# Optimization experiments

Measured on AMD Instinct MI355X. Metric: run time of the kernel, lower is better.

The kernel has to match this reference:

```python
import jax, jax.numpy as jnp
import numpy as np

D_MODEL = 1024
NUM_HEADS = 16
HEAD_DIM = D_MODEL // NUM_HEADS


def setup_inputs() -> dict:
    key = jax.random.key(0)
    ks = jax.random.split(key, 11)
    S, B, D = 2048, 2, D_MODEL
    scale = 1.0 / np.sqrt(D)
    inp = {
        'query': jax.random.normal(ks[0], (S, B, D), dtype=jnp.float32),
        'key': jax.random.normal(ks[1], (S, B, D), dtype=jnp.float32),
        'value': jax.random.normal(ks[2], (S, B, D), dtype=jnp.float32),
        'Wq': jax.random.normal(ks[3], (D, D), dtype=jnp.float32) * scale,
        'bq': jnp.zeros((D,), dtype=jnp.float32),
        'Wk': jax.random.normal(ks[4], (D, D), dtype=jnp.float32) * scale,
        'bk': jnp.zeros((D,), dtype=jnp.float32),
        'Wv': jax.random.normal(ks[5], (D, D), dtype=jnp.float32) * scale,
        'bv': jnp.zeros((D,), dtype=jnp.float32),
        'Wo': jax.random.normal(ks[6], (D, D), dtype=jnp.float32) * scale,
        'bo': jnp.zeros((D,), dtype=jnp.float32),
    }
    return inp


def reference(query, key, value, Wq, bq, Wk, bk, Wv, bv, Wo, bo):
    # query/key/value: [S, B, D] (seq-first, as in the torch module)
    S, B, D = query.shape
    H, Hd = NUM_HEADS, HEAD_DIM
    # Linear: x @ W.T + b (torch convention), then split heads -> [B, H, S, Hd]
    def proj_heads(x, W, b):
        y = jnp.einsum('sbd,ed->sbe', x, W) + b  # [S, B, D]
        return y.reshape(x.shape[0], B, H, Hd).transpose(1, 2, 0, 3)
    q = proj_heads(query, Wq, bq)   # [B, H, S, Hd]
    k = proj_heads(key, Wk, bk)     # [B, H, Sk, Hd]
    v = proj_heads(value, Wv, bv)   # [B, H, Sk, Hd]
    scores = jnp.einsum('bhsd,bhtd->bhst', q, k) / jnp.sqrt(jnp.asarray(Hd, q.dtype))
    probs = jax.nn.softmax(scores, axis=-1)  # dropout p=0.0 -> identity
    attn = jnp.einsum('bhst,bhtd->bhsd', probs, v)  # [B, H, S, Hd]
    attn = attn.transpose(2, 0, 1, 3).reshape(S, B, D)  # [S, B, D]
    out = jnp.einsum('sbd,ed->sbe', attn, Wo) + bo
    return out
```

## Files before the change

kernel.cpp:

```cpp
#include <hip/hip_runtime.h>
#include <stdint.h>

#define S_LEN 2048
#define BATCH 2
#define DM    1024
#define NH    16
#define HD    64
#define MROWS 4096

typedef float f32x4 __attribute__((ext_vector_type(4)));
typedef short bfrag __attribute__((ext_vector_type(8)));
typedef unsigned short u16x4_t __attribute__((ext_vector_type(4)));
typedef unsigned short u16x8_t __attribute__((ext_vector_type(8)));
typedef int i32x4_t __attribute__((ext_vector_type(4)));

#define EXP2F(x) __builtin_amdgcn_exp2f(x)

__device__ inline f32x4 mfma16(bfrag a, bfrag b, f32x4 c) {
    return __builtin_amdgcn_mfma_f32_16x16x32_bf16(a, b, c, 0, 0, 0);
}

__device__ inline unsigned short bf16_rn(float x) {
    unsigned u = __builtin_bit_cast(unsigned, x);
    return (unsigned short)((u + 0x7fffu + ((u >> 16) & 1u)) >> 16);
}

__device__ inline void split_bf16(float x, unsigned short &h, unsigned short &l) {
    unsigned u = __builtin_bit_cast(unsigned, x);
    h = (unsigned short)(u >> 16);
    float hf = __builtin_bit_cast(float, u & 0xffff0000u);
    float r = x - hf;
    l = (unsigned short)(__builtin_bit_cast(unsigned, r) >> 16);
}

__device__ inline unsigned cvtpk_bf16(float lo, float hi) {
    unsigned r;
    asm("v_cvt_pk_bf16_f32 %0, %1, %2" : "=v"(r) : "v"(lo), "v"(hi));
    return r;
}

__device__ inline void pl32swap(unsigned &a, unsigned &b) {
    asm("v_permlane32_swap_b32 %0, %1" : "+v"(a), "+v"(b));
}
__device__ inline void pl16swap(unsigned &a, unsigned &b) {
    asm("v_permlane16_swap_b32 %0, %1" : "+v"(a), "+v"(b));
}

typedef __attribute__((address_space(1))) const unsigned int as1_u32;
typedef __attribute__((address_space(3))) unsigned int as3_u32;
__device__ inline void async16(void* lds, const void* g) {
    __builtin_amdgcn_global_load_lds((as1_u32*)g, (as3_u32*)lds, 16, 0, 0);
}

__global__ __launch_bounds__(256)
void cvt_kernel(const float* __restrict__ Wq, const float* __restrict__ Wk,
                const float* __restrict__ Wv, const float* __restrict__ Wo,
                const float* __restrict__ Qin, const float* __restrict__ Kin,
                const float* __restrict__ Vin,
                unsigned short* __restrict__ Wqb, unsigned short* __restrict__ Wkb,
                unsigned short* __restrict__ Wvb,
                unsigned short* __restrict__ Woh, unsigned short* __restrict__ Wol,
                unsigned short* __restrict__ Qa,  unsigned short* __restrict__ Ka,
                unsigned short* __restrict__ Va)
{
    const int z = blockIdx.z;
    size_t idx = ((size_t)blockIdx.x * 256 + threadIdx.x) * 8;
    const size_t limit = (z < 4) ? (size_t)DM * DM : (size_t)MROWS * DM;
    if (idx >= limit) return;
    const float* src = (z == 0) ? Wq : (z == 1) ? Wk : (z == 2) ? Wv :
                       (z == 3) ? Wo : (z == 4) ? Qin : (z == 5) ? Kin : Vin;
    float4 f0 = *(const float4*)&src[idx];
    float4 f1 = *(const float4*)&src[idx + 4];
    if (z != 3) {
        unsigned short* dst = (z == 0) ? Wqb : (z == 1) ? Wkb : (z == 2) ? Wvb :
                              (z == 4) ? Qa  : (z == 5) ? Ka  : Va;
        u16x8_t v = { bf16_rn(f0.x), bf16_rn(f0.y), bf16_rn(f0.z), bf16_rn(f0.w),
                      bf16_rn(f1.x), bf16_rn(f1.y), bf16_rn(f1.z), bf16_rn(f1.w) };
        *(u16x8_t*)&dst[idx] = v;
    } else {
        unsigned short h0,h1,h2,h3,h4,h5,h6,h7, l0,l1,l2,l3,l4,l5,l6,l7;
        split_bf16(f0.x,h0,l0); split_bf16(f0.y,h1,l1);
        split_bf16(f0.z,h2,l2); split_bf16(f0.w,h3,l3);
        split_bf16(f1.x,h4,l4); split_bf16(f1.y,h5,l5);
        split_bf16(f1.z,h6,l6); split_bf16(f1.w,h7,l7);
        u16x8_t vh = {h0,h1,h2,h3,h4,h5,h6,h7};
        u16x8_t vl = {l0,l1,l2,l3,l4,l5,l6,l7};
        *(u16x8_t*)&Woh[idx] = vh;
        *(u16x8_t*)&Wol[idx] = vl;
    }
}

__global__ __launch_bounds__(256)
void qkv_gemm(const unsigned short* __restrict__ Qa,
              const unsigned short* __restrict__ Ka,
              const unsigned short* __restrict__ Va,
              const unsigned short* __restrict__ Wqb,
              const unsigned short* __restrict__ Wkb,
              const unsigned short* __restrict__ Wvb,
              const float* __restrict__ bq, const float* __restrict__ bk,
              const float* __restrict__ bv,
              unsigned short* __restrict__ Qb, unsigned short* __restrict__ Kb,
              unsigned short* __restrict__ Vt)
{
    __shared__ unsigned short sA[128*32];
    __shared__ unsigned short sB[128*32];

    const int tid = threadIdx.x, lane = tid & 63, w4 = tid >> 6;
    const int m16 = lane & 15, q4 = lane >> 4;
    const int wr = w4 >> 1, wc = w4 & 1;
    const int z = blockIdx.z;

    int id = blockIdx.x + 8 * blockIdx.y;
    int j  = id >> 3;
    const int m0 = ((id & 7) * 4 + (j & 3)) * 128;
    const int n0 = (j >> 2) * 128;

    const unsigned short* A = (z == 0) ? Qa : (z == 1) ? Ka : Va;
    const unsigned short* W = (z == 0) ? Wqb : (z == 1) ? Wkb : Wvb;
    const float* bias = (z == 0) ? bq : (z == 1) ? bk : bv;
    unsigned short* outp = (z == 0) ? Qb : (z == 1) ? Kb : Vt;

    const int G1 = tid + 256;
    const int r0 = tid >> 2, g0 = (tid & 3) ^ ((r0 ^ (r0 >> 2)) & 3);
    const int r1 = G1  >> 2, g1 = (G1  & 3) ^ ((r1 ^ (r1 >> 2)) & 3);
    const char* gA0 = (const char*)A + (size_t)(m0 + r0) * 2048 + g0 * 16;
    const char* gA1 = (const char*)A + (size_t)(m0 + r1) * 2048 + g1 * 16;
    const char* gB0 = (const char*)W + (size_t)(n0 + r0) * 2048 + g0 * 16;
    const char* gB1 = (const char*)W + (size_t)(n0 + r1) * 2048 + g1 * 16;
    char* ldsA0 = (char*)sA + w4 * 1024;
    char* ldsA1 = (char*)sA + 4096 + w4 * 1024;
    char* ldsB0 = (char*)sB + w4 * 1024;
    char* ldsB1 = (char*)sB + 4096 + w4 * 1024;

    int offA[4], offB[4];
    #pragma unroll
    for (int rt = 0; rt < 4; rt++) {
        int r = wr * 64 + rt * 16 + m16;
        offA[rt] = r * 32 + ((q4 ^ ((r ^ (r >> 2)) & 3)) << 3);
    }
    #pragma unroll
    for (int ct = 0; ct < 4; ct++) {
        int r = wc * 64 + ct * 16 + m16;
        offB[ct] = r * 32 + ((q4 ^ ((r ^ (r >> 2)) & 3)) << 3);
    }

    f32x4 acc[4][4];
    const f32x4 zero4 = {0.f, 0.f, 0.f, 0.f};
    #pragma unroll
    for (int i = 0; i < 4; i++)
        #pragma unroll
        for (int jj = 0; jj < 4; jj++) acc[i][jj] = zero4;

    for (int k0 = 0; k0 < DM; k0 += 32) {
        async16(ldsA0, gA0);
        async16(ldsA1, gA1);
        async16(ldsB0, gB0);
        async16(ldsB1, gB1);
        gA0 += 64; gA1 += 64; gB0 += 64; gB1 += 64;
        __syncthreads();

        bfrag a[4], bb[4];
        #pragma unroll
        for (int rt = 0; rt < 4; rt++) a[rt]  = *(const bfrag*)&sA[offA[rt]];
        #pragma unroll
        for (int ct = 0; ct < 4; ct++) bb[ct] = *(const bfrag*)&sB[offB[ct]];

        #pragma unroll
        for (int rt = 0; rt < 4; rt++)
            #pragma unroll
            for (int ct = 0; ct < 4; ct++)
                acc[rt][ct] = mfma16(a[rt], bb[ct], acc[rt][ct]);
        __syncthreads();
    }

    const float SCALE = (z == 0) ? 0.18033688011112042f : 1.0f;
    #pragma unroll
    for (int rt = 0; rt < 4; rt++)
        #pragma unroll
        for (int ct = 0; ct < 4; ct++)
            #pragma unroll
            for (int reg = 0; reg < 4; reg++) {
                int r = m0 + wr * 64 + rt * 16 + q4 * 4 + reg;
                int c = n0 + wc * 64 + ct * 16 + m16;
                float v = (acc[rt][ct][reg] + bias[c]) * SCALE;
                int s = r >> 1, b = r & 1, hh = c >> 6, d = c & 63;
                unsigned short bv16 = bf16_rn(v);
                if (z == 2)
                    outp[((size_t)(b * NH + hh) * HD + d) * S_LEN + s] = bv16;
                else
                    outp[((size_t)(b * NH + hh) * S_LEN + s) * HD + d] = bv16;
            }
}

__global__ __launch_bounds__(256, 4)
void attn_kernel(const unsigned short* __restrict__ Qb,
                 const unsigned short* __restrict__ Kb,
                 const unsigned short* __restrict__ Vt,
                 unsigned short* __restrict__ Op,
                 float* __restrict__ Lp)
{
    __shared__ unsigned short sK[2][64*64];
    __shared__ unsigned short sV[2][64*64];

    const int tid = threadIdx.x, lane = tid & 63, w4 = tid >> 6;
    const int m16 = lane & 15, q4 = lane >> 4;

    int id = blockIdx.x;
    int xcd = id & 7, j = id >> 3;
    const int bh   = xcd * 4 + (j >> 5);
    const int rem  = j & 31;
    const int half = rem & 1;
    const int qc   = rem >> 1;
    const int qw   = qc * 128 + w4 * 32;
    const int tbase = half * (S_LEN / 2);

    const unsigned short* Qp = Qb + (size_t)bh * (S_LEN * HD);
    const unsigned short* Kp = Kb + (size_t)bh * (S_LEN * HD);
    const unsigned short* Vp = Vt + (size_t)bh * (S_LEN * HD);

    bfrag aq[2][2];
    #pragma unroll
    for (int nt = 0; nt < 2; nt++)
        #pragma unroll
        for (int kc = 0; kc < 2; kc++)
            aq[nt][kc] = *(const bfrag*)&Qp[(size_t)(qw + nt*16 + m16) * HD + kc*32 + q4*8];

    const int r0 = tid >> 3,         g0 = (tid & 7) ^ (r0 & 7);
    const int r1 = (tid + 256) >> 3, g1 = (tid & 7) ^ (r1 & 7);
    const char* gK0 = (const char*)Kp + (size_t)(tbase + r0) * 128 + g0 * 16;
    const char* gK1 = (const char*)Kp + (size_t)(tbase + r1) * 128 + g1 * 16;
    const char* gV0 = (const char*)Vp + (size_t)r0 * 4096 + tbase * 2 + g0 * 16;
    const char* gV1 = (const char*)Vp + (size_t)r1 * 4096 + tbase * 2 + g1 * 16;
    const int ldsw = w4 * 1024;

    const f32x4 zero4 = {0.f, 0.f, 0.f, 0.f};
    f32x4 O[2][4];
    float lp[2] = {0.f, 0.f};
    #pragma unroll
    for (int nt = 0; nt < 2; nt++)
        #pragma unroll
        for (int dt = 0; dt < 4; dt++) O[nt][dt] = zero4;

    async16((char*)sK[0] + ldsw,        gK0);
    async16((char*)sK[0] + 4096 + ldsw, gK1);
    async16((char*)sV[0] + ldsw,        gV0);
    async16((char*)sV[0] + 4096 + ldsw, gV1);

    const int NT = (S_LEN / 2) / 64;
    for (int it = 0; it < NT; it++) {
        const int bi = it & 1;
        __syncthreads();
        if (it + 1 < NT) {
            size_t ko = (size_t)(it + 1) * 8192, vo = (size_t)(it + 1) * 128;
            async16((char*)sK[bi^1] + ldsw,        gK0 + ko);
            async16((char*)sK[bi^1] + 4096 + ldsw, gK1 + ko);
            async16((char*)sV[bi^1] + ldsw,        gV0 + vo);
            async16((char*)sV[bi^1] + 4096 + ldsw, gV1 + vo);
        }

        const unsigned short* kb = sK[bi];
        const unsigned short* vb = sV[bi];

        bfrag ak[4][2];
        #pragma unroll
        for (int mt = 0; mt < 4; mt++) {
            int r = mt*16 + m16, s = r & 7;
            ak[mt][0] = *(const bfrag*)&kb[r*64 + ((q4     ^ s) << 3)];
            ak[mt][1] = *(const bfrag*)&kb[r*64 + (((4+q4) ^ s) << 3)];
        }

        bfrag bpv[2][2];
        #pragma unroll
        for (int nt = 0; nt < 2; nt++) {
            f32x4 Sc[4];
            #pragma unroll
            for (int mt = 0; mt < 4; mt++) {
                Sc[mt] = mfma16(ak[mt][0], aq[nt][0], zero4);
                Sc[mt] = mfma16(ak[mt][1], aq[nt][1], Sc[mt]);
            }
            unsigned u0[4], u1[4];
            #pragma unroll
            for (int mt = 0; mt < 4; mt++) {
                float p0 = EXP2F(Sc[mt][0]), p1 = EXP2F(Sc[mt][1]);
                float p2 = EXP2F(Sc[mt][2]), p3 = EXP2F(Sc[mt][3]);
                lp[nt] += (p0 + p1) + (p2 + p3);
                u0[mt] = cvtpk_bf16(p0, p1);
                u1[mt] = cvtpk_bf16(p2, p3);
            }
            #pragma unroll
            for (int kc = 0; kc < 2; kc++) {
                unsigned a0 = u0[2*kc], b0 = u0[2*kc+1];
                pl32swap(a0, b0);
                pl16swap(a0, b0);
                unsigned a1 = u1[2*kc], b1 = u1[2*kc+1];
                pl32swap(a1, b1);
                pl16swap(a1, b1);
                i32x4_t w = { (int)a0, (int)a1, (int)b0, (int)b1 };
                bpv[nt][kc] = __builtin_bit_cast(bfrag, w);
            }
        }

        bfrag av[4][2];
        #pragma unroll
        for (int dt = 0; dt < 4; dt++) {
            int r = dt*16 + m16, s = r & 7;
            av[dt][0] = *(const bfrag*)&vb[r*64 + ((q4     ^ s) << 3)];
            av[dt][1] = *(const bfrag*)&vb[r*64 + (((4+q4) ^ s) << 3)];
        }

        #pragma unroll
        for (int nt = 0; nt < 2; nt++)
            #pragma unroll
            for (int dt = 0; dt < 4; dt++) {
                O[nt][dt] = mfma16(av[dt][0], bpv[nt][0], O[nt][dt]);
                O[nt][dt] = mfma16(av[dt][1], bpv[nt][1], O[nt][dt]);
            }
    }

    const size_t OPH = (size_t)BATCH * NH * S_LEN * HD;
    unsigned short* Ob = Op + (size_t)half * OPH;
    float* Lb = Lp + (size_t)half * (BATCH * NH * S_LEN);
    #pragma unroll
    for (int nt = 0; nt < 2; nt++) {
        float l = lp[nt];
        l += __shfl_xor(l, 16);
        l += __shfl_xor(l, 32);
        int q = qw + nt*16 + m16;
        if (q4 == 0) Lb[(size_t)bh * S_LEN + q] = l;
        size_t rb = ((size_t)bh * S_LEN + q) * HD;
        #pragma unroll
        for (int dt = 0; dt < 4; dt++) {
            u16x4_t o = { bf16_rn(O[nt][dt][0]), bf16_rn(O[nt][dt][1]),
                          bf16_rn(O[nt][dt][2]), bf16_rn(O[nt][dt][3]) };
            *(u16x4_t*)&Ob[rb + dt*16 + q4*4] = o;
        }
    }
}

__global__ __launch_bounds__(256)
void cmb_kernel(const unsigned short* __restrict__ Op,
                const float* __restrict__ Lp,
                unsigned short* __restrict__ Ap)
{
    const size_t OPH = (size_t)BATCH * NH * S_LEN * HD;
    int idx = blockIdx.x * 256 + threadIdx.x;
    int rho = idx >> 3, dg = idx & 7;
    size_t e = (size_t)rho * HD + dg * 8;
    float inv = 1.0f / (Lp[rho] + Lp[BATCH*NH*S_LEN + rho]);
    u16x8_t a = *(const u16x8_t*)&Op[e];
    u16x8_t b2 = *(const u16x8_t*)&Op[OPH + e];
    u16x8_t r;
    #pragma unroll
    for (int i = 0; i < 8; i++) {
        float fa = __builtin_bit_cast(float, (unsigned)(unsigned short)a[i]  << 16);
        float fb = __builtin_bit_cast(float, (unsigned)(unsigned short)b2[i] << 16);
        r[i] = bf16_rn((fa + fb) * inv);
    }
    int bh = rho >> 11, q = rho & 2047;
    int b = bh >> 4, h = bh & 15;
    *(u16x8_t*)&Ap[((size_t)(q * 2 + b)) * DM + h * 64 + dg * 8] = r;
}

__global__ __launch_bounds__(256)
void out_gemm(const unsigned short* __restrict__ Ap,
              const unsigned short* __restrict__ Woh,
              const unsigned short* __restrict__ Wol,
              const float* __restrict__ bo, float* __restrict__ out)
{
    __shared__ unsigned short sA[128*32];
    __shared__ unsigned short sH[64*32];
    __shared__ unsigned short sL[64*32];

    const int tid = threadIdx.x, lane = tid & 63, w4 = tid >> 6;
    const int m16 = lane & 15, q4 = lane >> 4;
    const int wr = w4 >> 1, wc = w4 & 1;

    int id = blockIdx.x + 16 * blockIdx.y;
    int j  = id >> 3;
    const int m0 = ((id & 7) * 4 + (j & 3)) * 128;
    const int n0 = (j >> 2) * 64;

    const int G1 = tid + 256;
    const int r0 = tid >> 2, g0 = (tid & 3) ^ ((r0 ^ (r0 >> 2)) & 3);
    const int r1 = G1  >> 2, g1 = (G1  & 3) ^ ((r1 ^ (r1 >> 2)) & 3);
    const char* gA0 = (const char*)Ap  + (size_t)(m0 + r0) * 2048 + g0 * 16;
    const char* gA1 = (const char*)Ap  + (size_t)(m0 + r1) * 2048 + g1 * 16;
    const char* gH  = (const char*)Woh + (size_t)(n0 + r0) * 2048 + g0 * 16;
    const char* gL  = (const char*)Wol + (size_t)(n0 + r0) * 2048 + g0 * 16;
    char* ldsA0 = (char*)sA + w4 * 1024;
    char* ldsA1 = (char*)sA + 4096 + w4 * 1024;
    char* ldsH  = (char*)sH + w4 * 1024;
    char* ldsL  = (char*)sL + w4 * 1024;

    int offA[4], offB[2];
    #pragma unroll
    for (int rt = 0; rt < 4; rt++) {
        int r = wr * 64 + rt * 16 + m16;
        offA[rt] = r * 32 + ((q4 ^ ((r ^ (r >> 2)) & 3)) << 3);
    }
    #pragma unroll
    for (int ct = 0; ct < 2; ct++) {
        int r = wc * 32 + ct * 16 + m16;
        offB[ct] = r * 32 + ((q4 ^ ((r ^ (r >> 2)) & 3)) << 3);
    }

    f32x4 acc[4][2];
    const f32x4 zero4 = {0.f, 0.f, 0.f, 0.f};
    #pragma unroll
    for (int i = 0; i < 4; i++)
        #pragma unroll
        for (int jj = 0; jj < 2; jj++) acc[i][jj] = zero4;

    for (int k0 = 0; k0 < DM; k0 += 32) {
        async16(ldsA0, gA0);
        async16(ldsA1, gA1);
        async16(ldsH,  gH);
        async16(ldsL,  gL);
        gA0 += 64; gA1 += 64; gH += 64; gL += 64;
        __syncthreads();

        bfrag a[4], bh2[2], bl2[2];
        #pragma unroll
        for (int rt = 0; rt < 4; rt++) a[rt] = *(const bfrag*)&sA[offA[rt]];
        #pragma unroll
        for (int ct = 0; ct < 2; ct++) {
            bh2[ct] = *(const bfrag*)&sH[offB[ct]];
            bl2[ct] = *(const bfrag*)&sL[offB[ct]];
        }
        #pragma unroll
        for (int rt = 0; rt < 4; rt++)
            #pragma unroll
            for (int ct = 0; ct < 2; ct++) {
                acc[rt][ct] = mfma16(a[rt], bh2[ct], acc[rt][ct]);
                acc[rt][ct] = mfma16(a[rt], bl2[ct], acc[rt][ct]);
            }
        __syncthreads();
    }

    #pragma unroll
    for (int rt = 0; rt < 4; rt++)
        #pragma unroll
        for (int ct = 0; ct < 2; ct++)
            #pragma unroll
            for (int reg = 0; reg < 4; reg++) {
                int r = m0 + wr * 64 + rt * 16 + q4 * 4 + reg;
                int c = n0 + wc * 32 + ct * 16 + m16;
                out[(size_t)r * DM + c] = acc[rt][ct][reg] + bo[c];
            }
}

extern "C" void kernel_launch(void* const* d_in, const int* in_sizes, int n_in,
                              void* d_out, int out_size, void* d_ws, size_t ws_size,
                              hipStream_t stream)
{
    const float* query = (const float*)d_in[0];
    const float* key   = (const float*)d_in[1];
    const float* value = (const float*)d_in[2];
    const float* Wq    = (const float*)d_in[3];
    const float* bq    = (const float*)d_in[4];
    const float* Wk    = (const float*)d_in[5];
    const float* bk    = (const float*)d_in[6];
    const float* Wv    = (const float*)d_in[7];
    const float* bv    = (const float*)d_in[8];
    const float* Wo    = (const float*)d_in[9];
    const float* bo    = (const float*)d_in[10];

    char* ws = (char*)d_ws;
    const size_t MB = 1u << 20;
    unsigned short* Qb  = (unsigned short*)(ws);
    unsigned short* Kb  = (unsigned short*)(ws +  8*MB);
    unsigned short* Vt  = (unsigned short*)(ws + 16*MB);
    unsigned short* Woh = (unsigned short*)(ws + 24*MB);
    unsigned short* Wol = (unsigned short*)(ws + 26*MB);
    unsigned short* Wqb = (unsigned short*)(ws + 28*MB);
    unsigned short* Wkb = (unsigned short*)(ws + 30*MB);
    unsigned short* Wvb = (unsigned short*)(ws + 32*MB);
    unsigned short* Va  = (unsigned short*)(ws + 34*MB);
    float*          Lp  = (float*)         (ws + 28*MB);
    unsigned short* Apl = (unsigned short*)(ws + 34*MB);
    unsigned short* Opart = (unsigned short*)d_out;
    unsigned short* Qa  = (unsigned short*)d_out;
    unsigned short* Ka  = (unsigned short*)d_out + (size_t)MROWS*DM;

    cvt_kernel<<<dim3(2048, 1, 7), 256, 0, stream>>>(
        Wq, Wk, Wv, Wo, query, key, value,
        Wqb, Wkb, Wvb, Woh, Wol, Qa, Ka, Va);
    qkv_gemm<<<dim3(8, 32, 3), 256, 0, stream>>>(
        Qa, Ka, Va, Wqb, Wkb, Wvb, bq, bk, bv, Qb, Kb, Vt);
    attn_kernel<<<dim3(1024), 256, 0, stream>>>(Qb, Kb, Vt, Opart, Lp);
    cmb_kernel<<<dim3(2048), 256, 0, stream>>>(Opart, Lp, Apl);
    out_gemm<<<dim3(16, 32), 256, 0, stream>>>(Apl, Woh, Wol, bo, (float*)d_out);
}
```

Before: 228.4 us.

## Split attention key range four ways and raise wave priority around MFMA blocks

Templates the attention and combine kernels on the number of key-range splits and, when workspace is large enough, uses four splits with twice as many blocks. The goal is more parallelism and better occupancy across CUs, since the earlier two-way split gave only 1024 blocks. It also wraps the MFMA sections in s_setprio to favour matrix work in scheduling. The cost is more partial-output traffic and a heavier combine pass, and which path runs depends on the workspace size.

```diff
diff --git a/kernel.cpp b/kernel.cpp
--- a/kernel.cpp
+++ b/kernel.cpp
@@ -192,11 +192,13 @@
             }
 }
 
+template<int TS>
 __global__ __launch_bounds__(256, 4)
 void attn_kernel(const unsigned short* __restrict__ Qb,
                  const unsigned short* __restrict__ Kb,
                  const unsigned short* __restrict__ Vt,
-                 unsigned short* __restrict__ Op,
+                 unsigned short* __restrict__ Op01,
+                 unsigned short* __restrict__ Op23,
                  float* __restrict__ Lp)
 {
     __shared__ unsigned short sK[2][64*64];
@@ -207,12 +209,14 @@
 
     int id = blockIdx.x;
     int xcd = id & 7, j = id >> 3;
-    const int bh   = xcd * 4 + (j >> 5);
-    const int rem  = j & 31;
-    const int half = rem & 1;
-    const int qc   = rem >> 1;
+    const int PER  = 16 * TS;
+    const int bh   = xcd * 4 + j / PER;
+    const int rem  = j % PER;
+    const int part = rem % TS;
+    const int qc   = rem / TS;
     const int qw   = qc * 128 + w4 * 32;
-    const int tbase = half * (S_LEN / 2);
+    const int TLEN = S_LEN / TS;
+    const int tbase = part * TLEN;
 
     const unsigned short* Qp = Qb + (size_t)bh * (S_LEN * HD);
     const unsigned short* Kp = Kb + (size_t)bh * (S_LEN * HD);
@@ -246,7 +250,7 @@
     async16((char*)sV[0] + ldsw,        gV0);
     async16((char*)sV[0] + 4096 + ldsw, gV1);
 
-    const int NT = (S_LEN / 2) / 64;
+    const int NT = TLEN / 64;
     for (int it = 0; it < NT; it++) {
         const int bi = it & 1;
         __syncthreads();
@@ -273,11 +277,13 @@
         #pragma unroll
         for (int nt = 0; nt < 2; nt++) {
             f32x4 Sc[4];
+            __builtin_amdgcn_s_setprio(1);
             #pragma unroll
             for (int mt = 0; mt < 4; mt++) {
                 Sc[mt] = mfma16(ak[mt][0], aq[nt][0], zero4);
                 Sc[mt] = mfma16(ak[mt][1], aq[nt][1], Sc[mt]);
             }
+            __builtin_amdgcn_s_setprio(0);
             unsigned u0[4], u1[4];
             #pragma unroll
             for (int mt = 0; mt < 4; mt++) {
@@ -308,6 +314,7 @@
             av[dt][1] = *(const bfrag*)&vb[r*64 + (((4+q4) ^ s) << 3)];
         }
 
+        __builtin_amdgcn_s_setprio(1);
         #pragma unroll
         for (int nt = 0; nt < 2; nt++)
             #pragma unroll
@@ -315,11 +322,13 @@
                 O[nt][dt] = mfma16(av[dt][0], bpv[nt][0], O[nt][dt]);
                 O[nt][dt] = mfma16(av[dt][1], bpv[nt][1], O[nt][dt]);
             }
+        __builtin_amdgcn_s_setprio(0);
     }
 
     const size_t OPH = (size_t)BATCH * NH * S_LEN * HD;
-    unsigned short* Ob = Op + (size_t)half * OPH;
-    float* Lb = Lp + (size_t)half * (BATCH * NH * S_LEN);
+    unsigned short* Ob = (part < 2) ? Op01 + (size_t)part * OPH
+                                    : Op23 + (size_t)(part - 2) * OPH;
+    float* Lb = Lp + (size_t)part * (BATCH * NH * S_LEN);
     #pragma unroll
     for (int nt = 0; nt < 2; nt++) {
         float l = lp[nt];
@@ -337,25 +346,35 @@
     }
 }
 
+template<int TS>
 __global__ __launch_bounds__(256)
-void cmb_kernel(const unsigned short* __restrict__ Op,
+void cmb_kernel(const unsigned short* __restrict__ Op01,
+                const unsigned short* __restrict__ Op23,
                 const float* __restrict__ Lp,
                 unsigned short* __restrict__ Ap)
 {
     const size_t OPH = (size_t)BATCH * NH * S_LEN * HD;
+    const int BNS = BATCH * NH * S_LEN;
     int idx = blockIdx.x * 256 + threadIdx.x;
     int rho = idx >> 3, dg = idx & 7;
     size_t e = (size_t)rho * HD + dg * 8;
-    float inv = 1.0f / (Lp[rho] + Lp[BATCH*NH*S_LEN + rho]);
-    u16x8_t a = *(const u16x8_t*)&Op[e];
-    u16x8_t b2 = *(const u16x8_t*)&Op[OPH + e];
+    float ls = 0.f;
+    #pragma unroll
+    for (int t = 0; t < TS; t++) ls += Lp[(size_t)t * BNS + rho];
+    float inv = 1.0f / ls;
+    float acc[8] = {0.f,0.f,0.f,0.f,0.f,0.f,0.f,0.f};
+    #pragma unroll
+    for (int t = 0; t < TS; t++) {
+        const unsigned short* src = (t < 2) ? Op01 + (size_t)t * OPH
+                                            : Op23 + (size_t)(t - 2) * OPH;
+        u16x8_t v = *(const u16x8_t*)&src[e];
+        #pragma unroll
+        for (int i = 0; i < 8; i++)
+            acc[i] += __builtin_bit_cast(float, (unsigned)(unsigned short)v[i] << 16);
+    }
     u16x8_t r;
     #pragma unroll
-    for (int i = 0; i < 8; i++) {
-        float fa = __builtin_bit_cast(float, (unsigned)(unsigned short)a[i]  << 16);
-        float fb = __builtin_bit_cast(float, (unsigned)(unsigned short)b2[i] << 16);
-        r[i] = bf16_rn((fa + fb) * inv);
-    }
+    for (int i = 0; i < 8; i++) r[i] = bf16_rn(acc[i] * inv);
     int bh = rho >> 11, q = rho & 2047;
     int b = bh >> 4, h = bh & 15;
     *(u16x8_t*)&Ap[((size_t)(q * 2 + b)) * DM + h * 64 + dg * 8] = r;
@@ -477,7 +496,9 @@
     unsigned short* Wvb = (unsigned short*)(ws + 32*MB);
     unsigned short* Va  = (unsigned short*)(ws + 34*MB);
     float*          Lp  = (float*)         (ws + 28*MB);
-    unsigned short* Apl = (unsigned short*)(ws + 34*MB);
+    unsigned short* Op23= (unsigned short*)(ws + 30*MB);
+    unsigned short* Apl2= (unsigned short*)(ws + 34*MB);
+    unsigned short* Apl4= (unsigned short*)(ws);
     unsigned short* Opart = (unsigned short*)d_out;
     unsigned short* Qa  = (unsigned short*)d_out;
     unsigned short* Ka  = (unsigned short*)d_out + (size_t)MROWS*DM;
@@ -487,7 +508,15 @@
         Wqb, Wkb, Wvb, Woh, Wol, Qa, Ka, Va);
     qkv_gemm<<<dim3(8, 32, 3), 256, 0, stream>>>(
         Qa, Ka, Va, Wqb, Wkb, Wvb, bq, bk, bv, Qb, Kb, Vt);
-    attn_kernel<<<dim3(1024), 256, 0, stream>>>(Qb, Kb, Vt, Opart, Lp);
-    cmb_kernel<<<dim3(2048), 256, 0, stream>>>(Opart, Lp, Apl);
-    out_gemm<<<dim3(16, 32), 256, 0, stream>>>(Apl, Woh, Wol, bo, (float*)d_out);
-}
+
+    const bool big = ws_size >= (size_t)46 * MB;
+    if (big) {
+        attn_kernel<4><<<dim3(2048), 256, 0, stream>>>(Qb, Kb, Vt, Opart, Op23, Lp);
+        cmb_kernel<4><<<dim3(2048), 256, 0, stream>>>(Opart, Op23, Lp, Apl4);
+        out_gemm<<<dim3(16, 32), 256, 0, stream>>>(Apl4, Woh, Wol, bo, (float*)d_out);
+    } else {
+        attn_kernel<2><<<dim3(1024), 256, 0, stream>>>(Qb, Kb, Vt, Opart, Opart, Lp);
+        cmb_kernel<2><<<dim3(2048), 256, 0, stream>>>(Opart, Opart, Lp, Apl2);
+        out_gemm<<<dim3(16, 32), 256, 0, stream>>>(Apl2, Woh, Wol, bo, (float*)d_out);
+    }
+}
```

New measurement: 250.9 us. 9.8% more time.

## Double-buffer LDS tiles in QKV and output GEMMs to overlap loads with MFMA

Applied to the files above, without the earlier changes.

Both projection GEMMs now keep two LDS buffers for the A and B tiles. The first k-tile is prefetched before the loop, and each iteration issues the async global-to-LDS copy for the next tile before running MFMAs on the current one. This hides global load latency behind compute and removes one of the two barriers per k-step. It doubles the LDS footprint per block, which could lower occupancy.

```diff
diff --git a/kernel.cpp b/kernel.cpp
--- a/kernel.cpp
+++ b/kernel.cpp
@@ -102,8 +102,8 @@
               unsigned short* __restrict__ Qb, unsigned short* __restrict__ Kb,
               unsigned short* __restrict__ Vt)
 {
-    __shared__ unsigned short sA[128*32];
-    __shared__ unsigned short sB[128*32];
+    __shared__ unsigned short sA[2][128*32];
+    __shared__ unsigned short sB[2][128*32];
 
     const int tid = threadIdx.x, lane = tid & 63, w4 = tid >> 6;
     const int m16 = lane & 15, q4 = lane >> 4;
@@ -127,10 +127,7 @@
     const char* gA1 = (const char*)A + (size_t)(m0 + r1) * 2048 + g1 * 16;
     const char* gB0 = (const char*)W + (size_t)(n0 + r0) * 2048 + g0 * 16;
     const char* gB1 = (const char*)W + (size_t)(n0 + r1) * 2048 + g1 * 16;
-    char* ldsA0 = (char*)sA + w4 * 1024;
-    char* ldsA1 = (char*)sA + 4096 + w4 * 1024;
-    char* ldsB0 = (char*)sB + w4 * 1024;
-    char* ldsB1 = (char*)sB + 4096 + w4 * 1024;
+    const int ldsw = w4 * 1024;
 
     int offA[4], offB[4];
     #pragma unroll
@@ -151,26 +148,34 @@
         #pragma unroll
         for (int jj = 0; jj < 4; jj++) acc[i][jj] = zero4;
 
-    for (int k0 = 0; k0 < DM; k0 += 32) {
-        async16(ldsA0, gA0);
-        async16(ldsA1, gA1);
-        async16(ldsB0, gB0);
-        async16(ldsB1, gB1);
-        gA0 += 64; gA1 += 64; gB0 += 64; gB1 += 64;
+    async16((char*)sA[0] + ldsw,        gA0);
+    async16((char*)sA[0] + 4096 + ldsw, gA1);
+    async16((char*)sB[0] + ldsw,        gB0);
+    async16((char*)sB[0] + 4096 + ldsw, gB1);
+
+    const int NK = DM / 32;
+    for (int it = 0; it < NK; it++) {
+        const int bi = it & 1;
         __syncthreads();
+        if (it + 1 < NK) {
+            size_t off = (size_t)(it + 1) * 64;
+            async16((char*)sA[bi^1] + ldsw,        gA0 + off);
+            async16((char*)sA[bi^1] + 4096 + ldsw, gA1 + off);
+            async16((char*)sB[bi^1] + ldsw,        gB0 + off);
+            async16((char*)sB[bi^1] + 4096 + ldsw, gB1 + off);
+        }
 
         bfrag a[4], bb[4];
         #pragma unroll
-        for (int rt = 0; rt < 4; rt++) a[rt]  = *(const bfrag*)&sA[offA[rt]];
-        #pragma unroll
-        for (int ct = 0; ct < 4; ct++) bb[ct] = *(const bfrag*)&sB[offB[ct]];
+        for (int rt = 0; rt < 4; rt++) a[rt]  = *(const bfrag*)&sA[bi][offA[rt]];
+        #pragma unroll
+        for (int ct = 0; ct < 4; ct++) bb[ct] = *(const bfrag*)&sB[bi][offB[ct]];
 
         #pragma unroll
         for (int rt = 0; rt < 4; rt++)
             #pragma unroll
             for (int ct = 0; ct < 4; ct++)
                 acc[rt][ct] = mfma16(a[rt], bb[ct], acc[rt][ct]);
-        __syncthreads();
     }
 
     const float SCALE = (z == 0) ? 0.18033688011112042f : 1.0f;
@@ -367,9 +372,9 @@
               const unsigned short* __restrict__ Wol,
               const float* __restrict__ bo, float* __restrict__ out)
 {
-    __shared__ unsigned short sA[128*32];
-    __shared__ unsigned short sH[64*32];
-    __shared__ unsigned short sL[64*32];
+    __shared__ unsigned short sA[2][128*32];
+    __shared__ unsigned short sH[2][64*32];
+    __shared__ unsigned short sL[2][64*32];
 
     const int tid = threadIdx.x, lane = tid & 63, w4 = tid >> 6;
     const int m16 = lane & 15, q4 = lane >> 4;
@@ -387,10 +392,7 @@
     const char* gA1 = (const char*)Ap  + (size_t)(m0 + r1) * 2048 + g1 * 16;
     const char* gH  = (const char*)Woh + (size_t)(n0 + r0) * 2048 + g0 * 16;
     const char* gL  = (const char*)Wol + (size_t)(n0 + r0) * 2048 + g0 * 16;
-    char* ldsA0 = (char*)sA + w4 * 1024;
-    char* ldsA1 = (char*)sA + 4096 + w4 * 1024;
-    char* ldsH  = (char*)sH + w4 * 1024;
-    char* ldsL  = (char*)sL + w4 * 1024;
+    const int ldsw = w4 * 1024;
 
     int offA[4], offB[2];
     #pragma unroll
@@ -411,21 +413,30 @@
         #pragma unroll
         for (int jj = 0; jj < 2; jj++) acc[i][jj] = zero4;
 
-    for (int k0 = 0; k0 < DM; k0 += 32) {
-        async16(ldsA0, gA0);
-        async16(ldsA1, gA1);
-        async16(ldsH,  gH);
-        async16(ldsL,  gL);
-        gA0 += 64; gA1 += 64; gH += 64; gL += 64;
+    async16((char*)sA[0] + ldsw,        gA0);
+    async16((char*)sA[0] + 4096 + ldsw, gA1);
+    async16((char*)sH[0] + ldsw,        gH);
+    async16((char*)sL[0] + ldsw,        gL);
+
+    const int NK = DM / 32;
+    for (int it = 0; it < NK; it++) {
+        const int bi = it & 1;
         __syncthreads();
+        if (it + 1 < NK) {
+            size_t off = (size_t)(it + 1) * 64;
+            async16((char*)sA[bi^1] + ldsw,        gA0 + off);
+            async16((char*)sA[bi^1] + 4096 + ldsw, gA1 + off);
+            async16((char*)sH[bi^1] + ldsw,        gH  + off);
+            async16((char*)sL[bi^1] + ldsw,        gL  + off);
+        }
 
         bfrag a[4], bh2[2], bl2[2];
         #pragma unroll
-        for (int rt = 0; rt < 4; rt++) a[rt] = *(const bfrag*)&sA[offA[rt]];
+        for (int rt = 0; rt < 4; rt++) a[rt] = *(const bfrag*)&sA[bi][offA[rt]];
         #pragma unroll
         for (int ct = 0; ct < 2; ct++) {
-            bh2[ct] = *(const bfrag*)&sH[offB[ct]];
-            bl2[ct] = *(const bfrag*)&sL[offB[ct]];
+            bh2[ct] = *(const bfrag*)&sH[bi][offB[ct]];
+            bl2[ct] = *(const bfrag*)&sL[bi][offB[ct]];
         }
         #pragma unroll
         for (int rt = 0; rt < 4; rt++)
@@ -434,7 +445,6 @@
                 acc[rt][ct] = mfma16(a[rt], bh2[ct], acc[rt][ct]);
                 acc[rt][ct] = mfma16(a[rt], bl2[ct], acc[rt][ct]);
             }
-        __syncthreads();
     }
 
     #pragma unroll
```

After: 235.6 us. +3.1%, slower.
